# Kernel tuning notes

Measured on AMD Instinct MI355X. Metric: run time of the kernel, lower is better.

## Reference

```python
import jax, jax.numpy as jnp
import numpy as np

F = 128          # feature_size
N = 512          # num_vertices (batch_size fixed to 1 by the original indexing)
C = 32 * 7 * 7 * 7   # 10976, f2 channel dim
G = 13           # f2 spatial grid (indices = (v+1)*6 in [0,12])
EPS = 1e-5


def _block(x, W1, b1, W2, b2, g, be, m, v):
    # Linear -> ELU -> Linear -> ELU -> Dropout(eval=id) -> BatchNorm1d(eval)
    h = jax.nn.elu(x @ W1 + b1)
    h = jax.nn.elu(h @ W2 + b2)
    return (h - m) * (g * jax.lax.rsqrt(v + EPS)) + be


def setup_inputs() -> dict:
    key = jax.random.key(0)
    ks = iter(jax.random.split(key, 80))

    def nrm(sh, s):
        return jax.random.normal(next(ks), sh, jnp.float32) * s

    def lin(i, o):
        return nrm((i, o), 1.0 / np.sqrt(i)), nrm((o,), 0.01)

    def bn():
        g = 1.0 + nrm((F,), 0.05)
        be = nrm((F,), 0.05)
        m = nrm((F,), 0.1)
        v = jax.random.uniform(next(ks), (F,), jnp.float32) + 0.5
        return g, be, m, v

    d = {}
    d['vertices'] = jax.random.uniform(next(ks), (1, N, 3), jnp.float32) * 2.0 - 1.0
    d['f2'] = nrm((1, G, G, G, C), 0.1)
    ii = jnp.arange(N, dtype=jnp.int32)
    d['v1s_idx'] = jnp.repeat(ii, N)   # edge k=(i,j): i = k//N
    d['v2s_idx'] = jnp.tile(ii, N)     #               j = k%N
    d['adj'] = (jax.random.uniform(next(ks), (N, N)) < 0.05).astype(jnp.float32)

    for p, (i, o) in [('mv', (3, F)), ('mf', (C, F)), ('s1', (2 * F, F)),
                      ('s2', (F, F)), ('s3', (2 * F, F))]:
        W1, b1 = lin(i, o)
        W2, b2 = lin(F, F)
        g, be, m, v = bn()
        d.update({p + '_W1': W1, p + '_b1': b1, p + '_W2': W2, p + '_b2': b2,
                  p + '_g': g, p + '_be': be, p + '_m': m, p + '_v': v})
    W3, b3 = lin(F, 2)
    d['s3_W3'], d['s3_b3'] = W3, b3
    return d


def _forward(vertices, f2, adj,
             mv_W1, mv_b1, mv_W2, mv_b2, mv_g, mv_be, mv_m, mv_v,
             mf_W1, mf_b1, mf_W2, mf_b2, mf_g, mf_be, mf_m, mf_v,
             s1_W1, s1_b1, s1_W2, s1_b2, s1_g, s1_be, s1_m, s1_v,
             s2_W1, s2_b1, s2_W2, s2_b2, s2_g, s2_be, s2_m, s2_v,
             s3_W1, s3_b1, s3_W2, s3_b2, s3_g, s3_be, s3_m, s3_v, s3_W3, s3_b3,
             v1s_idx, v2s_idx):
    b, n, _ = vertices.shape
    flat = vertices.reshape(-1, 3)                        # (B*N, 3)
    idx = ((flat + 1.0) * 6.0).astype(jnp.int32)          # grid indices in [0,12]
    f2e = f2[0, idx[:, 0], idx[:, 1], idx[:, 2], :]       # gather: (B*N, C)
    vf = _block(flat, mv_W1, mv_b1, mv_W2, mv_b2, mv_g, mv_be, mv_m, mv_v)
    ff = _block(f2e, mf_W1, mf_b1, mf_W2, mf_b2, mf_g, mf_be, mf_m, mf_v)
    vert = jnp.concatenate([vf, ff], -1).reshape(b, n, 2 * F)  # (B, N, 2F)

    # stage1: NodeToEdge (endpoint combine) -> MLP block over all N^2 edges
    e1 = vert[:, v1s_idx] + vert[:, v2s_idx]              # (B, N*N, 2F)
    s1 = _block(e1, s1_W1, s1_b1, s1_W2, s1_b2, s1_g, s1_be, s1_m, s1_v)  # (B, E, F)

    # stage2: EdgeToNode (adjacency-masked sum) -> MLP -> NodeToEdge
    nodes = jnp.einsum('bijf,ij->bif', s1.reshape(b, n, n, F), adj)  # (B, N, F)
    n2 = _block(nodes, s2_W1, s2_b1, s2_W2, s2_b2, s2_g, s2_be, s2_m, s2_v)
    s2 = n2[:, v1s_idx] + n2[:, v2s_idx]                  # (B, E, F)

    cat = jnp.concatenate([s1, s2], -1).reshape(b * n * n, 2 * F)
    h = _block(cat, s3_W1, s3_b1, s3_W2, s3_b2, s3_g, s3_be, s3_m, s3_v)
    return (h @ s3_W3 + s3_b3).reshape(b, n, n, 2)


def reference(vertices, f2, v1s_idx, v2s_idx, adj,
              mv_W1, mv_b1, mv_W2, mv_b2, mv_g, mv_be, mv_m, mv_v,
              mf_W1, mf_b1, mf_W2, mf_b2, mf_g, mf_be, mf_m, mf_v,
              s1_W1, s1_b1, s1_W2, s1_b2, s1_g, s1_be, s1_m, s1_v,
              s2_W1, s2_b1, s2_W2, s2_b2, s2_g, s2_be, s2_m, s2_v,
              s3_W1, s3_b1, s3_W2, s3_b2, s3_g, s3_be, s3_m, s3_v, s3_W3, s3_b3):
    return _forward(vertices, f2, adj,
                    mv_W1, mv_b1, mv_W2, mv_b2, mv_g, mv_be, mv_m, mv_v,
                    mf_W1, mf_b1, mf_W2, mf_b2, mf_g, mf_be, mf_m, mf_v,
                    s1_W1, s1_b1, s1_W2, s1_b2, s1_g, s1_be, s1_m, s1_v,
                    s2_W1, s2_b1, s2_W2, s2_b2, s2_g, s2_be, s2_m, s2_v,
                    s3_W1, s3_b1, s3_W2, s3_b2, s3_g, s3_be, s3_m, s3_v, s3_W3, s3_b3,
                    v1s_idx, v2s_idx)
```

## Files before the change

kernel.cpp:

```cpp
#include <hip/hip_runtime.h>
#include <hip/hip_bf16.h>


#define F    128
#define NV   512
#define CCC  10976
#define EPSV 1e-5f

typedef __attribute__((ext_vector_type(8)))  short        short8;
typedef __attribute__((ext_vector_type(4)))  float        f32x4;
typedef __attribute__((ext_vector_type(4)))  float        flt4;
typedef __attribute__((ext_vector_type(4)))  unsigned int u32x4;

union Frag { u32x4 q; short8 s; unsigned int d[4]; unsigned short u[8]; };

__device__ __forceinline__ unsigned short f2bf(float x){
  union { float f; unsigned int u; } c; c.f = x;
  unsigned int r = c.u + 0x7FFFu + ((c.u >> 16) & 1u);
  return (unsigned short)(r >> 16);
}
__device__ __forceinline__ unsigned int pkbf(float a, float b){
  union { __hip_bfloat162 h; unsigned int u; } cv;
  cv.h = __float22bfloat162_rn(make_float2(a, b));
  return cv.u;
}
__device__ __forceinline__ float eluf(float x){
  return x > 0.f ? x : (__expf(x) - 1.f);
}
__device__ __forceinline__ f32x4 mfma16(short8 a, short8 b, f32x4 c){
  return __builtin_amdgcn_mfma_f32_16x16x32_bf16(a, b, c, 0, 0, 0);
}

#define WS_U      0u
#define WS_FFPRE  262144u
#define WS_WPERM  524288u
#define WS_CTR    786432u
#define WS_VEC    794624u
#define WS_W2FS1  799744u
#define WS_W1AFS3 832512u
#define WS_W2FS3  865280u
#define WS_W3F    898048u
#define WS_MFW1F  902144u
#define WS_END    3712000u
#define WS_PART   3712000u
#define WS_PART_END 14984192u


#define NJOBS   4352
#define NSTATIC 4096

__global__ __launch_bounds__(256) void k_setup(
    const float* s1W2, const float* s3W1, const float* s3W2, const float* s3W3,
    const float* __restrict__ mfW1,
    const float* s1g, const float* s1v,
    const float* s3g, const float* s3be, const float* s3m, const float* s3v,
    const float* s1be, const float* s1m,
    const float* s1b2, const float* s3b2,
    unsigned short* w2fs1, unsigned short* w1afs3, unsigned short* w2fs3,
    unsigned short* w3f, unsigned short* __restrict__ mfw1f,
    float* vec, float* zeroreg, unsigned int* ctr, int use_parts)
{
  __shared__ float sm[32 * 132];
  int bid = blockIdx.x, tid = threadIdx.x;
  if (bid == 0 && tid < 8) ctr[tid * 256] = 0u;

  if (bid < 460){
    int t = bid * 256 + tid;
    if (t < 49152){
      int T = t >> 14, tt = t & 16383;
      int e = tt & 7, lane = (tt >> 3) & 63, grp = tt >> 9;
      int slot = (grp >> 3) * 32 + ((lane >> 4) & 3) * 8 + e;
      int col  = (grp & 7) * 16 + (lane & 15);
      float val;
      unsigned short* dst;
      if (T == 0){ dst = w2fs1; val = s1W2[slot * F + col]; }
      else {
        int kf = (slot & 7) * 16 + (slot >> 3);
        if (T == 1){
          float sc1 = s1g[kf] * rsqrtf(s1v[kf] + EPSV);
          dst = w1afs3; val = sc1 * s3W1[kf * F + col];
        } else {
          dst = w2fs3; val = s3W2[kf * F + col];
        }
      }
      dst[tt] = f2bf(val);
      return;
    }
    t -= 49152;
    if (t < 2048){
      int e = t & 7, lane = (t >> 3) & 63, ks = t >> 9;
      int slot = ks * 32 + ((lane >> 4) & 3) * 8 + e;
      int kf = (slot & 7) * 16 + (slot >> 3);
      int n = lane & 15;
      float sc3 = s3g[kf] * rsqrtf(s3v[kf] + EPSV);
      w3f[t] = f2bf(n < 2 ? sc3 * s3W3[kf * 2 + n] : 0.f);
      return;
    }
    t -= 2048;
    if (t < 1024){
      int f = t & 127, which = t >> 7;
      int s = (f & 15) * 8 + (f >> 4);
      switch (which){
        case 0: vec[512 + s] = s1b2[f]; break;
        case 1: vec[640 + s] = s3b2[f]; break;
        case 2: vec[768 + f] = s1g[f] * rsqrtf(s1v[f] + EPSV); break;
        case 3: vec[896 + f] = s1be[f] - s1m[f] * (s1g[f] * rsqrtf(s1v[f] + EPSV)); break;
        case 4: {
          float a = 0.f;
          for (int k = 0; k < F; ++k){
            float sc = s1g[k] * rsqrtf(s1v[k] + EPSV);
            a = fmaf(s1be[k] - s1m[k] * sc, s3W1[k * F + f], a);
          }
          vec[1024 + f] = a;
        } break;
        case 5: if (f < 16){
          float a = 0.f;
          if (f < 2){
            for (int k = 0; k < F; ++k){
              float sc = s3g[k] * rsqrtf(s3v[k] + EPSV);
              a = fmaf(s3be[k] - s3m[k] * sc, s3W3[k * 2 + f], a);
            }
          }
          vec[1152 + f] = a;
        } break;
        default: break;
      }
      return;
    }
    t -= 1024;
    if (t < 65536 && !use_parts) zeroreg[t] = 0.f;
    return;
  }

  {
    int ksg = bid - 460;
    const float* src = mfW1 + ksg * 32 * F;
    #pragma unroll
    for (int p = 0; p < 4; ++p){
      int g4 = tid + p * 256;
      int row = g4 >> 5, col = (g4 & 31) * 4;
      flt4 v = *(const flt4*)(src + row * F + col);
      *(flt4*)(sm + row * 132 + col) = v;
    }
    __syncthreads();
    unsigned int* dst = (unsigned int*)mfw1f + ksg * 2048;
    #pragma unroll
    for (int q2 = 0; q2 < 8; ++q2){
      int o = (tid * 8 + q2) * 2;
      int nt = o >> 9, lane = (o >> 3) & 63, e = o & 7;
      int k = (lane >> 4) * 8 + e;
      int n = nt * 16 + (lane & 15);
      dst[tid * 8 + q2] = pkbf(sm[k * 132 + n], sm[(k + 1) * 132 + n]);
    }
  }
}

__global__ __launch_bounds__(256) void k_ff1(
    const float* __restrict__ verts, const float* __restrict__ f2,
    const unsigned short* __restrict__ mfw1f, float* __restrict__ ffpre,
    float* __restrict__ partials, int use_parts)
{
  int tid = threadIdx.x, w = tid >> 6, l = tid & 63, g = l >> 4, mm = l & 15;
  int mb = blockIdx.x & 7, kc = blockIdx.x >> 3;
  int v = mb * 64 + w * 16 + mm;
  float x0 = verts[v * 3 + 0], x1 = verts[v * 3 + 1], x2 = verts[v * 3 + 2];
  int i0 = (int)((x0 + 1.f) * 6.f), i1 = (int)((x1 + 1.f) * 6.f), i2 = (int)((x2 + 1.f) * 6.f);
  int base = ((i0 * 13 + i1) * 13 + i2) * CCC;

  f32x4 zero = {0.f, 0.f, 0.f, 0.f};
  f32x4 acc[8];
  #pragma unroll
  for (int nt = 0; nt < 8; ++nt) acc[nt] = zero;

  const u32x4* bt = (const u32x4*)mfw1f;
  int kmax = 343 - kc * 8; if (kmax > 8) kmax = 8;
  for (int kk = 0; kk < kmax; ++kk){
    int ksg = kc * 8 + kk;
    const float* ap = f2 + base + ksg * 32 + g * 8;
    flt4 a0 = *(const flt4*)ap;
    flt4 a1 = *(const flt4*)(ap + 4);
    Frag a;
    a.d[0] = pkbf(a0.x, a0.y); a.d[1] = pkbf(a0.z, a0.w);
    a.d[2] = pkbf(a1.x, a1.y); a.d[3] = pkbf(a1.z, a1.w);
    #pragma unroll
    for (int nt = 0; nt < 8; ++nt){
      Frag b; b.q = bt[(ksg * 8 + nt) * 64 + l];
      acc[nt] = mfma16(a.s, b.s, acc[nt]);
    }
  }
  if (use_parts){
    #pragma unroll
    for (int nt = 0; nt < 8; ++nt){
      int n = nt * 16 + mm;
      #pragma unroll
      for (int r = 0; r < 4; ++r)
        partials[(kc * NV + mb * 64 + w * 16 + g * 4 + r) * F + n] = acc[nt][r];
    }
  } else {
    #pragma unroll
    for (int nt = 0; nt < 8; ++nt){
      int n = nt * 16 + mm;
      #pragma unroll
      for (int r = 0; r < 4; ++r)
        atomicAdd(&ffpre[(mb * 64 + w * 16 + g * 4 + r) * F + n], acc[nt][r]);
    }
  }
}

__global__ __launch_bounds__(256) void k_vert(
    const float* __restrict__ verts, const float* __restrict__ ffpre,
    const float* __restrict__ partials, int use_parts,
    const float* mvW1, const float* mvb1, const float* mvW2, const float* mvb2,
    const float* mvg, const float* mvbe, const float* mvm, const float* mvv,
    const float* mfb1, const float* mfW2, const float* mfb2,
    const float* mfg, const float* mfbe, const float* mfm, const float* mfv,
    const float* s1W1, const float* s1b1, float* __restrict__ uP)
{
  __shared__ float hv[F], hf[F], vf[F], ff[F], ph0[F], ph1[F];
  int tid = threadIdx.x, f = tid & 127, half = tid >> 7, v = blockIdx.x;
  if (half == 0){
    float x0 = verts[v * 3], x1 = verts[v * 3 + 1], x2 = verts[v * 3 + 2];
    hv[f] = eluf(mvb1[f] + x0 * mvW1[f] + x1 * mvW1[F + f] + x2 * mvW1[2 * F + f]);
  } else {
    float fp;
    if (use_parts){
      fp = 0.f;
      for (int kc = 0; kc < 43; ++kc) fp += partials[(kc * NV + v) * F + f];
    } else {
      fp = ffpre[v * F + f];
    }
    hf[f] = eluf(fp + mfb1[f]);
  }
  __syncthreads();
  {
    float psv = 0.f, psf = 0.f;
    const float* wv_ = mvW2 + half * 64 * F + f;
    const float* wf_ = mfW2 + half * 64 * F + f;
    const float* hvk = hv + half * 64;
    const float* hfk = hf + half * 64;
    for (int k = 0; k < 64; ++k){
      psv = fmaf(hvk[k], wv_[k * F], psv);
      psf = fmaf(hfk[k], wf_[k * F], psf);
    }
    if (half){ ph0[f] = psv; ph1[f] = psf; }
    __syncthreads();
    if (!half){
      float sv = mvb2[f] + psv + ph0[f];
      float sf = mfb2[f] + psf + ph1[f];
      vf[f] = (eluf(sv) - mvm[f]) * (mvg[f] * rsqrtf(mvv[f] + EPSV)) + mvbe[f];
      ff[f] = (eluf(sf) - mfm[f]) * (mfg[f] * rsqrtf(mfv[f] + EPSV)) + mfbe[f];
    }
    __syncthreads();
  }
  {
    float pu = 0.f;
    if (half == 0){
      for (int k = 0; k < F; ++k) pu = fmaf(vf[k], s1W1[k * F + f], pu);
    } else {
      for (int k = 0; k < F; ++k) pu = fmaf(ff[k], s1W1[(128 + k) * F + f], pu);
    }
    if (half) ph0[f] = pu;
    __syncthreads();
    if (!half) uP[v * F + f] = 0.5f * s1b1[f] + pu + ph0[f];
  }
}

__global__ __launch_bounds__(256) void k_pass1m(
    const float* __restrict__ uP, const unsigned short* __restrict__ w2fs1,
    const float* __restrict__ vec, const float* __restrict__ adj,
    const float* s2W1, const float* s2b1, const float* s2W2, const float* s2b2,
    const float* s2g, const float* s2be, const float* s2m, const float* s2v,
    const float* s3W1, const float* s3b1, float* __restrict__ wPp)
{
  __shared__ u32x4 Wb[2048];
  __shared__ float ci[F], nblk[F], bb[F], mh0[F];
  __shared__ unsigned short pjl[128];
  __shared__ unsigned long long msk[8];
  int tid = threadIdx.x, i = blockIdx.x;
  int wv = tid >> 6, ln = tid & 63;

  bool p0 = adj[i * NV + tid] != 0.f;
  bool p1 = adj[i * NV + 256 + tid] != 0.f;
  unsigned long long m0 = __ballot(p0);
  unsigned long long m1 = __ballot(p1);
  if (ln == 0){ msk[wv] = m0; msk[4 + wv] = m1; }
  { const u32x4* ws_ = (const u32x4*)w2fs1;
    #pragma unroll
    for (int ii = 0; ii < 8; ++ii) Wb[tid + 256 * ii] = ws_[tid + 256 * ii]; }
  if (tid < F){ ci[tid] = uP[i * F + tid]; nblk[tid] = 0.f; }
  __syncthreads();
  int base0 = 0, base1 = 0, tot = 0;
  #pragma unroll
  for (int g = 0; g < 8; ++g){
    int c = __popcll(msk[g]);
    if (g < wv) base0 += c;
    if (g < 4 + wv) base1 += c;
    tot += c;
  }
  unsigned long long below = (1ull << ln) - 1ull;
  if (p0){
    int r = base0 + __popcll(m0 & below);
    if (r < 128) pjl[r] = (unsigned short)tid;
  }
  if (p1){
    int r = base1 + __popcll(m1 & below);
    if (r < 128) pjl[r] = (unsigned short)(256 + tid);
  }
  int cnt = tot > 128 ? 128 : tot;
  float cntf = (float)tot;
  __syncthreads();

  int w = tid >> 6, l = tid & 63, g = l >> 4, mm = l & 15;
  float b2v[8];
  *(flt4*)&b2v[0] = *(const flt4*)(vec + 512 + mm * 8);
  *(flt4*)&b2v[4] = *(const flt4*)(vec + 516 + mm * 8);

  for (int t = 0; t * 64 < cnt; ++t){
    int row = t * 64 + w * 16 + mm;
    int j = (row < cnt) ? (int)pjl[row] : 0;
    f32x4 acc[8];
    #pragma unroll
    for (int nt = 0; nt < 8; ++nt){ float b = b2v[nt]; acc[nt] = (f32x4){b, b, b, b}; }
    #pragma unroll
    for (int ks = 0; ks < 4; ++ks){
      int kb = ks * 32 + g * 8;
      flt4 ua = *(const flt4*)(uP + j * F + kb);
      flt4 ub = *(const flt4*)(uP + j * F + kb + 4);
      flt4 c0 = *(const flt4*)&ci[kb];
      flt4 c1 = *(const flt4*)&ci[kb + 4];
      Frag a;
      a.d[0] = pkbf(eluf(ua.x + c0.x), eluf(ua.y + c0.y));
      a.d[1] = pkbf(eluf(ua.z + c0.z), eluf(ua.w + c0.w));
      a.d[2] = pkbf(eluf(ub.x + c1.x), eluf(ub.y + c1.y));
      a.d[3] = pkbf(eluf(ub.z + c1.z), eluf(ub.w + c1.w));
      #pragma unroll
      for (int nt = 0; nt < 8; ++nt){
        Frag b; b.q = Wb[(ks * 8 + nt) * 64 + l];
        acc[nt] = mfma16(a.s, b.s, acc[nt]);
      }
    }
    int rbase = t * 64 + w * 16 + g * 4;
    float mk[4];
    #pragma unroll
    for (int r = 0; r < 4; ++r) mk[r] = (rbase + r < cnt) ? 1.f : 0.f;
    #pragma unroll
    for (int nt = 0; nt < 8; ++nt){
      float s = mk[0] * eluf(acc[nt][0]);
      s = fmaf(mk[1], eluf(acc[nt][1]), s);
      s = fmaf(mk[2], eluf(acc[nt][2]), s);
      s = fmaf(mk[3], eluf(acc[nt][3]), s);
      s += __shfl_xor(s, 16, 64);
      s += __shfl_xor(s, 32, 64);
      if (l < 16) atomicAdd(&nblk[nt * 16 + mm], s);
    }
  }
  __syncthreads();

  if (tid < F) ci[tid] = vec[768 + tid] * nblk[tid] + vec[896 + tid] * cntf;
  __syncthreads();
  int f = tid & 127, half = tid >> 7;
  {
    float p = 0.f;
    const float* Wc = s2W1 + half * 64 * F + f;
    const float* av = ci + half * 64;
    for (int k = 0; k < 64; ++k) p = fmaf(av[k], Wc[k * F], p);
    if (half) mh0[f] = p;
    __syncthreads();
    if (!half) bb[f] = eluf(s2b1[f] + p + mh0[f]);
    __syncthreads();
  }
  {
    float p = 0.f;
    const float* Wc = s2W2 + half * 64 * F + f;
    const float* av = bb + half * 64;
    for (int k = 0; k < 64; ++k) p = fmaf(av[k], Wc[k * F], p);
    if (half) mh0[f] = p;
    __syncthreads();
    if (!half){
      float s2 = s2b2[f] + p + mh0[f];
      nblk[f] = (eluf(s2) - s2m[f]) * (s2g[f] * rsqrtf(s2v[f] + EPSV)) + s2be[f];
    }
    __syncthreads();
  }
  {
    float p = 0.f;
    const float* Wc = s3W1 + (128 + half * 64) * F + f;
    const float* av = nblk + half * 64;
    for (int k = 0; k < 64; ++k) p = fmaf(av[k], Wc[k * F], p);
    if (half) mh0[f] = p;
    __syncthreads();
    if (!half){
      float wvv = 0.5f * (s3b1[f] + vec[1024 + f]) + p + mh0[f];
      wPp[i * F + ((f & 15) * 8 + (f >> 4))] = wvv;
    }
  }
}

__global__ __launch_bounds__(512, 2) void k_pass3(
    const float* __restrict__ uP, const float* __restrict__ wPp,
    const unsigned short* __restrict__ w2fs1, const unsigned short* __restrict__ w1afs3,
    const unsigned short* __restrict__ w2fs3, const unsigned short* __restrict__ w3f,
    const float* __restrict__ vec, const float* __restrict__ s3b3,
    unsigned int* __restrict__ ctr, float* __restrict__ out)
{
  __shared__ u32x4 Wall[6144];
  __shared__ __align__(16) char Hb[65536];
  int tid = threadIdx.x;
  {
    const u32x4* p0 = (const u32x4*)w2fs1;
    const u32x4* p1 = (const u32x4*)w1afs3;
    const u32x4* p2 = (const u32x4*)w2fs3;
    #pragma unroll
    for (int ii = 0; ii < 4; ++ii){
      Wall[       tid + 512 * ii] = p0[tid + 512 * ii];
      Wall[2048 + tid + 512 * ii] = p1[tid + 512 * ii];
      Wall[4096 + tid + 512 * ii] = p2[tid + 512 * ii];
    }
  }
  __syncthreads();

  int w = tid >> 6, l = tid & 63, g = l >> 4, mm = l & 15;
  char* hb = Hb + w * 8192;
  int sx = (mm & 7) << 4;
  int wgid = blockIdx.x * 8 + w;
  unsigned int* ctrp = ctr + (blockIdx.x & 7) * 256;
  int cgrp = blockIdx.x & 7;

  float b2v1[8], b2v3[8];
  *(flt4*)&b2v1[0] = *(const flt4*)(vec + 512 + mm * 8);
  *(flt4*)&b2v1[4] = *(const flt4*)(vec + 516 + mm * 8);
  *(flt4*)&b2v3[0] = *(const flt4*)(vec + 640 + mm * 8);
  *(flt4*)&b2v3[4] = *(const flt4*)(vec + 644 + mm * 8);
  float bb = (mm < 2) ? (s3b3[mm] + vec[1152 + mm]) : 0.f;
  Frag w3r[4];
  #pragma unroll
  for (int ks = 0; ks < 4; ++ks) w3r[ks].q = ((const u32x4*)w3f)[ks * 64 + l];

  int phase = 0;
  for (;;){
    int id;
    if (phase < 2){
      id = wgid * 2 + phase;
      ++phase;
    } else {
      int t;
      if (l == 0) t = (int)atomicAdd(ctrp, 1u);
      t = __shfl(t, 0, 64);
      if (t >= 32) break;
      id = NSTATIC + cgrp * 32 + t;
    }
    int q = (id >= 512) + (id >= 992) + (id >= 1440) + (id >= 1856)
          + (id >= 2240) + (id >= 2592) + (id >= 2912) + (id >= 3200)
          + (id >= 3456) + (id >= 3680) + (id >= 3872) + (id >= 4032)
          + (id >= 4160) + (id >= 4256) + (id >= 4320);
    int Sq = 32 * (16 * q - ((q * (q - 1)) >> 1));
    int r_ = id - Sq;
    int den = 16 - q;
    int i = q * 32 + r_ / den;
    int jbase = 32 * (q + r_ % den);

    flt4 c0[4], c1[4];
    #pragma unroll
    for (int ks = 0; ks < 4; ++ks){
      c0[ks] = *(const flt4*)(uP + i * F + ks * 32 + g * 8);
      c1[ks] = *(const flt4*)(uP + i * F + ks * 32 + g * 8 + 4);
    }

    f32x4 acc[2][8];
    #pragma unroll
    for (int m = 0; m < 2; ++m)
    #pragma unroll
    for (int nt = 0; nt < 8; ++nt){ float b = b2v1[nt]; acc[m][nt] = (f32x4){b, b, b, b}; }
    #pragma unroll
    for (int ks = 0; ks < 4; ++ks){
      int kb = ks * 32 + g * 8;
      Frag a0, a1;
      {
        const float* p0 = uP + (jbase + mm) * F + kb;
        flt4 ua = *(const flt4*)p0;
        flt4 ub = *(const flt4*)(p0 + 4);
        a0.d[0] = pkbf(eluf(ua.x + c0[ks].x), eluf(ua.y + c0[ks].y));
        a0.d[1] = pkbf(eluf(ua.z + c0[ks].z), eluf(ua.w + c0[ks].w));
        a0.d[2] = pkbf(eluf(ub.x + c1[ks].x), eluf(ub.y + c1[ks].y));
        a0.d[3] = pkbf(eluf(ub.z + c1[ks].z), eluf(ub.w + c1[ks].w));
        const float* p1 = uP + (jbase + 16 + mm) * F + kb;
        flt4 va = *(const flt4*)p1;
        flt4 vb = *(const flt4*)(p1 + 4);
        a1.d[0] = pkbf(eluf(va.x + c0[ks].x), eluf(va.y + c0[ks].y));
        a1.d[1] = pkbf(eluf(va.z + c0[ks].z), eluf(va.w + c0[ks].w));
        a1.d[2] = pkbf(eluf(vb.x + c1[ks].x), eluf(vb.y + c1[ks].y));
        a1.d[3] = pkbf(eluf(vb.z + c1[ks].z), eluf(vb.w + c1[ks].w));
      }
      #pragma unroll
      for (int nt = 0; nt < 8; ++nt){
        Frag b; b.q = Wall[(ks * 8 + nt) * 64 + l];
        acc[0][nt] = mfma16(a0.s, b.s, acc[0][nt]);
        acc[1][nt] = mfma16(a1.s, b.s, acc[1][nt]);
      }
    }
    #pragma unroll
    for (int m = 0; m < 2; ++m)
    #pragma unroll
    for (int r = 0; r < 4; ++r){
      int row = m * 16 + g * 4 + r;
      u32x4 wd;
      #pragma unroll
      for (int qq = 0; qq < 4; ++qq)
        wd[qq] = pkbf(eluf(acc[m][2*qq][r]), eluf(acc[m][2*qq+1][r]));
      *(u32x4*)(hb + row * 256 + ((mm * 16) ^ ((row & 7) << 4))) = wd;
    }

    {
      float wiv[8];
      *(flt4*)&wiv[0] = *(const flt4*)(wPp + i * F + mm * 8);
      *(flt4*)&wiv[4] = *(const flt4*)(wPp + i * F + mm * 8 + 4);
      #pragma unroll
      for (int m = 0; m < 2; ++m)
      #pragma unroll
      for (int nt = 0; nt < 8; ++nt){ float b = wiv[nt]; acc[m][nt] = (f32x4){b, b, b, b}; }
    }
    #pragma unroll
    for (int ks = 0; ks < 4; ++ks){
      Frag a0; a0.q = *(const u32x4*)(hb + mm * 256 + ((ks * 64 + g * 16) ^ sx));
      Frag a1; a1.q = *(const u32x4*)(hb + (16 + mm) * 256 + ((ks * 64 + g * 16) ^ sx));
      #pragma unroll
      for (int nt = 0; nt < 8; ++nt){
        Frag b; b.q = Wall[2048 + (ks * 8 + nt) * 64 + l];
        acc[0][nt] = mfma16(a0.s, b.s, acc[0][nt]);
        acc[1][nt] = mfma16(a1.s, b.s, acc[1][nt]);
      }
    }
    #pragma unroll
    for (int m = 0; m < 2; ++m)
    #pragma unroll
    for (int r = 0; r < 4; ++r){
      int row = m * 16 + g * 4 + r;
      int jj = jbase + row;
      float wjv[8];
      *(flt4*)&wjv[0] = *(const flt4*)(wPp + jj * F + mm * 8);
      *(flt4*)&wjv[4] = *(const flt4*)(wPp + jj * F + mm * 8 + 4);
      u32x4 wd;
      #pragma unroll
      for (int qq = 0; qq < 4; ++qq)
        wd[qq] = pkbf(eluf(acc[m][2*qq][r] + wjv[2*qq]), eluf(acc[m][2*qq+1][r] + wjv[2*qq+1]));
      *(u32x4*)(hb + row * 256 + ((mm * 16) ^ ((row & 7) << 4))) = wd;
    }

    #pragma unroll
    for (int m = 0; m < 2; ++m)
    #pragma unroll
    for (int nt = 0; nt < 8; ++nt){ float b = b2v3[nt]; acc[m][nt] = (f32x4){b, b, b, b}; }
    #pragma unroll
    for (int ks = 0; ks < 4; ++ks){
      Frag a0; a0.q = *(const u32x4*)(hb + mm * 256 + ((ks * 64 + g * 16) ^ sx));
      Frag a1; a1.q = *(const u32x4*)(hb + (16 + mm) * 256 + ((ks * 64 + g * 16) ^ sx));
      #pragma unroll
      for (int nt = 0; nt < 8; ++nt){
        Frag b; b.q = Wall[4096 + (ks * 8 + nt) * 64 + l];
        acc[0][nt] = mfma16(a0.s, b.s, acc[0][nt]);
        acc[1][nt] = mfma16(a1.s, b.s, acc[1][nt]);
      }
    }
    #pragma unroll
    for (int m = 0; m < 2; ++m)
    #pragma unroll
    for (int r = 0; r < 4; ++r){
      int row = m * 16 + g * 4 + r;
      u32x4 wd;
      #pragma unroll
      for (int qq = 0; qq < 4; ++qq)
        wd[qq] = pkbf(eluf(acc[m][2*qq][r]), eluf(acc[m][2*qq+1][r]));
      *(u32x4*)(hb + row * 256 + ((mm * 16) ^ ((row & 7) << 4))) = wd;
    }

    f32x4 acc4[2] = {{bb, bb, bb, bb}, {bb, bb, bb, bb}};
    #pragma unroll
    for (int ks = 0; ks < 4; ++ks){
      Frag a0; a0.q = *(const u32x4*)(hb + mm * 256 + ((ks * 64 + g * 16) ^ sx));
      Frag a1; a1.q = *(const u32x4*)(hb + (16 + mm) * 256 + ((ks * 64 + g * 16) ^ sx));
      acc4[0] = mfma16(a0.s, w3r[ks].s, acc4[0]);
      acc4[1] = mfma16(a1.s, w3r[ks].s, acc4[1]);
    }
    if (mm < 2){
      #pragma unroll
      for (int m = 0; m < 2; ++m)
      #pragma unroll
      for (int r = 0; r < 4; ++r){
        int jr = jbase + m * 16 + g * 4 + r;
        if (jr >= i){
          float val = acc4[m][r];
          out[(i * NV + jr) * 2 + mm] = val;
          out[(jr * NV + i) * 2 + mm] = val;
        }
      }
    }
  }
}

extern "C" void kernel_launch(void* const* d_in, const int* in_sizes, int n_in,
                              void* d_out, int out_size, void* d_ws, size_t ws_size,
                              hipStream_t stream)
{
  (void)in_sizes; (void)n_in; (void)out_size;
  const float* vertices = (const float*)d_in[0];
  const float* f2   = (const float*)d_in[1];
  const float* adj  = (const float*)d_in[4];
  const float* mvW1 = (const float*)d_in[5];
  const float* mvb1 = (const float*)d_in[6];
  const float* mvW2 = (const float*)d_in[7];
  const float* mvb2 = (const float*)d_in[8];
  const float* mvg  = (const float*)d_in[9];
  const float* mvbe = (const float*)d_in[10];
  const float* mvm  = (const float*)d_in[11];
  const float* mvv  = (const float*)d_in[12];
  const float* mfW1 = (const float*)d_in[13];
  const float* mfb1 = (const float*)d_in[14];
  const float* mfW2 = (const float*)d_in[15];
  const float* mfb2 = (const float*)d_in[16];
  const float* mfg  = (const float*)d_in[17];
  const float* mfbe = (const float*)d_in[18];
  const float* mfm  = (const float*)d_in[19];
  const float* mfv  = (const float*)d_in[20];
  const float* s1W1 = (const float*)d_in[21];
  const float* s1b1 = (const float*)d_in[22];
  const float* s1W2 = (const float*)d_in[23];
  const float* s1b2 = (const float*)d_in[24];
  const float* s1g  = (const float*)d_in[25];
  const float* s1be = (const float*)d_in[26];
  const float* s1m  = (const float*)d_in[27];
  const float* s1v  = (const float*)d_in[28];
  const float* s2W1 = (const float*)d_in[29];
  const float* s2b1 = (const float*)d_in[30];
  const float* s2W2 = (const float*)d_in[31];
  const float* s2b2 = (const float*)d_in[32];
  const float* s2g  = (const float*)d_in[33];
  const float* s2be = (const float*)d_in[34];
  const float* s2m  = (const float*)d_in[35];
  const float* s2v  = (const float*)d_in[36];
  const float* s3W1 = (const float*)d_in[37];
  const float* s3b1 = (const float*)d_in[38];
  const float* s3W2 = (const float*)d_in[39];
  const float* s3b2 = (const float*)d_in[40];
  const float* s3g  = (const float*)d_in[41];
  const float* s3be = (const float*)d_in[42];
  const float* s3m  = (const float*)d_in[43];
  const float* s3v  = (const float*)d_in[44];
  const float* s3W3 = (const float*)d_in[45];
  const float* s3b3 = (const float*)d_in[46];

  char* ws = (char*)d_ws;
  float* uP    = (float*)(ws + WS_U);
  float* ffpre = (float*)(ws + WS_FFPRE);
  float* wPp   = (float*)(ws + WS_WPERM);
  unsigned int* ctr = (unsigned int*)(ws + WS_CTR);
  float* vec   = (float*)(ws + WS_VEC);
  unsigned short* w2fs1  = (unsigned short*)(ws + WS_W2FS1);
  unsigned short* w1afs3 = (unsigned short*)(ws + WS_W1AFS3);
  unsigned short* w2fs3  = (unsigned short*)(ws + WS_W2FS3);
  unsigned short* w3f    = (unsigned short*)(ws + WS_W3F);
  unsigned short* mfw1f  = (unsigned short*)(ws + WS_MFW1F);
  float* parts = (float*)(ws + WS_PART);
  int use_parts = (ws_size >= (size_t)WS_PART_END) ? 1 : 0;

  k_setup<<<803, 256, 0, stream>>>(s1W2, s3W1, s3W2, s3W3, mfW1,
      s1g, s1v, s3g, s3be, s3m, s3v, s1be, s1m, s1b2, s3b2,
      w2fs1, w1afs3, w2fs3, w3f, mfw1f, vec, ffpre, ctr, use_parts);
  k_ff1<<<344, 256, 0, stream>>>(vertices, f2, mfw1f, ffpre, parts, use_parts);
  k_vert<<<512, 256, 0, stream>>>(vertices, ffpre, parts, use_parts,
      mvW1, mvb1, mvW2, mvb2, mvg, mvbe, mvm, mvv,
      mfb1, mfW2, mfb2, mfg, mfbe, mfm, mfv,
      s1W1, s1b1, uP);
  k_pass1m<<<512, 256, 0, stream>>>(uP, w2fs1, vec, adj,
      s2W1, s2b1, s2W2, s2b2, s2g, s2be, s2m, s2v, s3W1, s3b1, wPp);
  k_pass3<<<256, 512, 0, stream>>>(uP, wPp, w2fs1, w1afs3, w2fs3, w3f, vec,
      s3b3, ctr, (float*)d_out);
}
```

Before: 95.27 us.

## Fuse mfW1 bf16 conversion into ff1 and shrink pass3 tiles to 16 rows

```diff
diff --git a/kernel.cpp b/kernel.cpp
--- a/kernel.cpp
+++ b/kernel.cpp
@@ -40,126 +40,99 @@
 #define WS_W1AFS3 832512u
 #define WS_W2FS3  865280u
 #define WS_W3F    898048u
-#define WS_MFW1F  902144u
-#define WS_END    3712000u
-#define WS_PART   3712000u
-#define WS_PART_END 14984192u
-
-
-#define NJOBS   4352
-#define NSTATIC 4096
+#define WS_END    902144u
+#define WS_PART   902144u
+#define WS_PART_END 12174336u
+
+
+#define NJOBS16   8448
+#define NSTATIC16 6144
 
 __global__ __launch_bounds__(256) void k_setup(
     const float* s1W2, const float* s3W1, const float* s3W2, const float* s3W3,
-    const float* __restrict__ mfW1,
     const float* s1g, const float* s1v,
     const float* s3g, const float* s3be, const float* s3m, const float* s3v,
     const float* s1be, const float* s1m,
     const float* s1b2, const float* s3b2,
     unsigned short* w2fs1, unsigned short* w1afs3, unsigned short* w2fs3,
-    unsigned short* w3f, unsigned short* __restrict__ mfw1f,
-    float* vec, float* zeroreg, unsigned int* ctr, int use_parts)
+    unsigned short* w3f, float* vec, float* zeroreg, unsigned int* ctr,
+    int use_parts)
+{
+  int bid = blockIdx.x, tid = threadIdx.x;
+  if (bid == 0 && tid < 8) ctr[tid * 256] = 0u;
+
+  int t = bid * 256 + tid;
+  if (t < 49152){
+    int T = t >> 14, tt = t & 16383;
+    int e = tt & 7, lane = (tt >> 3) & 63, grp = tt >> 9;
+    int slot = (grp >> 3) * 32 + ((lane >> 4) & 3) * 8 + e;
+    int col  = (grp & 7) * 16 + (lane & 15);
+    float val;
+    unsigned short* dst;
+    if (T == 0){ dst = w2fs1; val = s1W2[slot * F + col]; }
+    else {
+      int kf = (slot & 7) * 16 + (slot >> 3);
+      if (T == 1){
+        float sc1 = s1g[kf] * rsqrtf(s1v[kf] + EPSV);
+        dst = w1afs3; val = sc1 * s3W1[kf * F + col];
+      } else {
+        dst = w2fs3; val = s3W2[kf * F + col];
+      }
+    }
+    dst[tt] = f2bf(val);
+    return;
+  }
+  t -= 49152;
+  if (t < 2048){
+    int e = t & 7, lane = (t >> 3) & 63, ks = t >> 9;
+    int slot = ks * 32 + ((lane >> 4) & 3) * 8 + e;
+    int kf = (slot & 7) * 16 + (slot >> 3);
+    int n = lane & 15;
+    float sc3 = s3g[kf] * rsqrtf(s3v[kf] + EPSV);
+    w3f[t] = f2bf(n < 2 ? sc3 * s3W3[kf * 2 + n] : 0.f);
+    return;
+  }
+  t -= 2048;
+  if (t < 1024){
+    int f = t & 127, which = t >> 7;
+    int s = (f & 15) * 8 + (f >> 4);
+    switch (which){
+      case 0: vec[512 + s] = s1b2[f]; break;
+      case 1: vec[640 + s] = s3b2[f]; break;
+      case 2: vec[768 + f] = s1g[f] * rsqrtf(s1v[f] + EPSV); break;
+      case 3: vec[896 + f] = s1be[f] - s1m[f] * (s1g[f] * rsqrtf(s1v[f] + EPSV)); break;
+      case 4: {
+        float a = 0.f;
+        for (int k = 0; k < F; ++k){
+          float sc = s1g[k] * rsqrtf(s1v[k] + EPSV);
+          a = fmaf(s1be[k] - s1m[k] * sc, s3W1[k * F + f], a);
+        }
+        vec[1024 + f] = a;
+      } break;
+      case 5: if (f < 16){
+        float a = 0.f;
+        if (f < 2){
+          for (int k = 0; k < F; ++k){
+            float sc = s3g[k] * rsqrtf(s3v[k] + EPSV);
+            a = fmaf(s3be[k] - s3m[k] * sc, s3W3[k * 2 + f], a);
+          }
+        }
+        vec[1152 + f] = a;
+      } break;
+      default: break;
+    }
+    return;
+  }
+  t -= 1024;
+  if (t < 65536 && !use_parts) zeroreg[t] = 0.f;
+}
+
+__global__ __launch_bounds__(256) void k_ff1(
+    const float* __restrict__ verts, const float* __restrict__ f2,
+    const float* __restrict__ mfW1, float* __restrict__ ffpre,
+    float* __restrict__ partials, int use_parts)
 {
   __shared__ float sm[32 * 132];
-  int bid = blockIdx.x, tid = threadIdx.x;
-  if (bid == 0 && tid < 8) ctr[tid * 256] = 0u;
-
-  if (bid < 460){
-    int t = bid * 256 + tid;
-    if (t < 49152){
-      int T = t >> 14, tt = t & 16383;
-      int e = tt & 7, lane = (tt >> 3) & 63, grp = tt >> 9;
-      int slot = (grp >> 3) * 32 + ((lane >> 4) & 3) * 8 + e;
-      int col  = (grp & 7) * 16 + (lane & 15);
-      float val;
-      unsigned short* dst;
-      if (T == 0){ dst = w2fs1; val = s1W2[slot * F + col]; }
-      else {
-        int kf = (slot & 7) * 16 + (slot >> 3);
-        if (T == 1){
-          float sc1 = s1g[kf] * rsqrtf(s1v[kf] + EPSV);
-          dst = w1afs3; val = sc1 * s3W1[kf * F + col];
-        } else {
-          dst = w2fs3; val = s3W2[kf * F + col];
-        }
-      }
-      dst[tt] = f2bf(val);
-      return;
-    }
-    t -= 49152;
-    if (t < 2048){
-      int e = t & 7, lane = (t >> 3) & 63, ks = t >> 9;
-      int slot = ks * 32 + ((lane >> 4) & 3) * 8 + e;
-      int kf = (slot & 7) * 16 + (slot >> 3);
-      int n = lane & 15;
-      float sc3 = s3g[kf] * rsqrtf(s3v[kf] + EPSV);
-      w3f[t] = f2bf(n < 2 ? sc3 * s3W3[kf * 2 + n] : 0.f);
-      return;
-    }
-    t -= 2048;
-    if (t < 1024){
-      int f = t & 127, which = t >> 7;
-      int s = (f & 15) * 8 + (f >> 4);
-      switch (which){
-        case 0: vec[512 + s] = s1b2[f]; break;
-        case 1: vec[640 + s] = s3b2[f]; break;
-        case 2: vec[768 + f] = s1g[f] * rsqrtf(s1v[f] + EPSV); break;
-        case 3: vec[896 + f] = s1be[f] - s1m[f] * (s1g[f] * rsqrtf(s1v[f] + EPSV)); break;
-        case 4: {
-          float a = 0.f;
-          for (int k = 0; k < F; ++k){
-            float sc = s1g[k] * rsqrtf(s1v[k] + EPSV);
-            a = fmaf(s1be[k] - s1m[k] * sc, s3W1[k * F + f], a);
-          }
-          vec[1024 + f] = a;
-        } break;
-        case 5: if (f < 16){
-          float a = 0.f;
-          if (f < 2){
-            for (int k = 0; k < F; ++k){
-              float sc = s3g[k] * rsqrtf(s3v[k] + EPSV);
-              a = fmaf(s3be[k] - s3m[k] * sc, s3W3[k * 2 + f], a);
-            }
-          }
-          vec[1152 + f] = a;
-        } break;
-        default: break;
-      }
-      return;
-    }
-    t -= 1024;
-    if (t < 65536 && !use_parts) zeroreg[t] = 0.f;
-    return;
-  }
-
-  {
-    int ksg = bid - 460;
-    const float* src = mfW1 + ksg * 32 * F;
-    #pragma unroll
-    for (int p = 0; p < 4; ++p){
-      int g4 = tid + p * 256;
-      int row = g4 >> 5, col = (g4 & 31) * 4;
-      flt4 v = *(const flt4*)(src + row * F + col);
-      *(flt4*)(sm + row * 132 + col) = v;
-    }
-    __syncthreads();
-    unsigned int* dst = (unsigned int*)mfw1f + ksg * 2048;
-    #pragma unroll
-    for (int q2 = 0; q2 < 8; ++q2){
-      int o = (tid * 8 + q2) * 2;
-      int nt = o >> 9, lane = (o >> 3) & 63, e = o & 7;
-      int k = (lane >> 4) * 8 + e;
-      int n = nt * 16 + (lane & 15);
-      dst[tid * 8 + q2] = pkbf(sm[k * 132 + n], sm[(k + 1) * 132 + n]);
-    }
-  }
-}
-
-__global__ __launch_bounds__(256) void k_ff1(
-    const float* __restrict__ verts, const float* __restrict__ f2,
-    const unsigned short* __restrict__ mfw1f, float* __restrict__ ffpre,
-    float* __restrict__ partials, int use_parts)
-{
   int tid = threadIdx.x, w = tid >> 6, l = tid & 63, g = l >> 4, mm = l & 15;
   int mb = blockIdx.x & 7, kc = blockIdx.x >> 3;
   int v = mb * 64 + w * 16 + mm;
@@ -172,10 +145,19 @@
   #pragma unroll
   for (int nt = 0; nt < 8; ++nt) acc[nt] = zero;
 
-  const u32x4* bt = (const u32x4*)mfw1f;
   int kmax = 343 - kc * 8; if (kmax > 8) kmax = 8;
+  int k0 = g * 8;
   for (int kk = 0; kk < kmax; ++kk){
     int ksg = kc * 8 + kk;
+    const float* src = mfW1 + ksg * 32 * F;
+    #pragma unroll
+    for (int p = 0; p < 4; ++p){
+      int g4 = tid + p * 256;
+      int row = g4 >> 5, col = (g4 & 31) * 4;
+      flt4 vv = *(const flt4*)(src + row * F + col);
+      *(flt4*)(sm + row * 132 + col) = vv;
+    }
+    __syncthreads();
     const float* ap = f2 + base + ksg * 32 + g * 8;
     flt4 a0 = *(const flt4*)ap;
     flt4 a1 = *(const flt4*)(ap + 4);
@@ -184,9 +166,14 @@
     a.d[2] = pkbf(a1.x, a1.y); a.d[3] = pkbf(a1.z, a1.w);
     #pragma unroll
     for (int nt = 0; nt < 8; ++nt){
-      Frag b; b.q = bt[(ksg * 8 + nt) * 64 + l];
+      int n = nt * 16 + mm;
+      Frag b;
+      #pragma unroll
+      for (int j = 0; j < 4; ++j)
+        b.d[j] = pkbf(sm[(k0 + 2 * j) * 132 + n], sm[(k0 + 2 * j + 1) * 132 + n]);
       acc[nt] = mfma16(a.s, b.s, acc[nt]);
     }
+    __syncthreads();
   }
   if (use_parts){
     #pragma unroll
@@ -396,7 +383,7 @@
   }
 }
 
-__global__ __launch_bounds__(512, 2) void k_pass3(
+__global__ __launch_bounds__(768, 3) void k_pass3(
     const float* __restrict__ uP, const float* __restrict__ wPp,
     const unsigned short* __restrict__ w2fs1, const unsigned short* __restrict__ w1afs3,
     const unsigned short* __restrict__ w2fs3, const unsigned short* __restrict__ w3f,
@@ -404,25 +391,28 @@
     unsigned int* __restrict__ ctr, float* __restrict__ out)
 {
   __shared__ u32x4 Wall[6144];
-  __shared__ __align__(16) char Hb[65536];
+  __shared__ __align__(16) char Hb[49152];
   int tid = threadIdx.x;
   {
     const u32x4* p0 = (const u32x4*)w2fs1;
     const u32x4* p1 = (const u32x4*)w1afs3;
     const u32x4* p2 = (const u32x4*)w2fs3;
     #pragma unroll
-    for (int ii = 0; ii < 4; ++ii){
-      Wall[       tid + 512 * ii] = p0[tid + 512 * ii];
-      Wall[2048 + tid + 512 * ii] = p1[tid + 512 * ii];
-      Wall[4096 + tid + 512 * ii] = p2[tid + 512 * ii];
+    for (int ii = 0; ii < 3; ++ii){
+      int idx = tid + 768 * ii;
+      if (idx < 2048){
+        Wall[idx]        = p0[idx];
+        Wall[2048 + idx] = p1[idx];
+        Wall[4096 + idx] = p2[idx];
+      }
     }
   }
   __syncthreads();
 
   int w = tid >> 6, l = tid & 63, g = l >> 4, mm = l & 15;
-  char* hb = Hb + w * 8192;
+  char* hb = Hb + w * 4096;
   int sx = (mm & 7) << 4;
-  int wgid = blockIdx.x * 8 + w;
+  int wgid = blockIdx.x * 12 + w;
   unsigned int* ctrp = ctr + (blockIdx.x & 7) * 256;
   int cgrp = blockIdx.x & 7;
 
@@ -431,7 +421,7 @@
   *(flt4*)&b2v1[4] = *(const flt4*)(vec + 516 + mm * 8);
   *(flt4*)&b2v3[0] = *(const flt4*)(vec + 640 + mm * 8);
   *(flt4*)&b2v3[4] = *(const flt4*)(vec + 644 + mm * 8);
-  float bb = (mm < 2) ? (s3b3[mm] + vec[1152 + mm]) : 0.f;
+  float bbc = (mm < 2) ? (s3b3[mm] + vec[1152 + mm]) : 0.f;
   Frag w3r[4];
   #pragma unroll
   for (int ks = 0; ks < 4; ++ks) w3r[ks].q = ((const u32x4*)w3f)[ks * 64 + l];
@@ -446,149 +436,132 @@
       int t;
       if (l == 0) t = (int)atomicAdd(ctrp, 1u);
       t = __shfl(t, 0, 64);
-      if (t >= 32) break;
-      id = NSTATIC + cgrp * 32 + t;
-    }
-    int q = (id >= 512) + (id >= 992) + (id >= 1440) + (id >= 1856)
-          + (id >= 2240) + (id >= 2592) + (id >= 2912) + (id >= 3200)
-          + (id >= 3456) + (id >= 3680) + (id >= 3872) + (id >= 4032)
-          + (id >= 4160) + (id >= 4256) + (id >= 4320);
-    int Sq = 32 * (16 * q - ((q * (q - 1)) >> 1));
-    int r_ = id - Sq;
-    int den = 16 - q;
-    int i = q * 32 + r_ / den;
-    int jbase = 32 * (q + r_ % den);
-
-    flt4 c0[4], c1[4];
+      if (t >= 288) break;
+      id = NSTATIC16 + cgrp * 288 + t;
+    }
+    int gq = (int)((65.0f - sqrtf(4225.0f - 0.5f * (float)id)) * 0.5f);
+    if (gq < 0) gq = 0; if (gq > 31) gq = 31;
+    while (gq < 31 && 8 * (gq + 1) * (65 - (gq + 1)) <= id) ++gq;
+    while (gq > 0 && 8 * gq * (65 - gq) > id) --gq;
+    int r_ = id - 8 * gq * (65 - gq);
+    int den = 32 - gq;
+    int i = gq * 16 + r_ / den;
+    int jbase = 16 * (gq + r_ % den);
+
+    flt4 c0[4], c1[4], u0[4], u1[4];
     #pragma unroll
     for (int ks = 0; ks < 4; ++ks){
       c0[ks] = *(const flt4*)(uP + i * F + ks * 32 + g * 8);
       c1[ks] = *(const flt4*)(uP + i * F + ks * 32 + g * 8 + 4);
-    }
-
-    f32x4 acc[2][8];
-    #pragma unroll
-    for (int m = 0; m < 2; ++m)
-    #pragma unroll
-    for (int nt = 0; nt < 8; ++nt){ float b = b2v1[nt]; acc[m][nt] = (f32x4){b, b, b, b}; }
+      const float* pA = uP + (jbase + mm) * F + ks * 32 + g * 8;
+      u0[ks] = *(const flt4*)pA;
+      u1[ks] = *(const flt4*)(pA + 4);
+    }
+
+    f32x4 acc[8];
+    #pragma unroll
+    for (int nt = 0; nt < 8; ++nt){ float b = b2v1[nt]; acc[nt] = (f32x4){b, b, b, b}; }
     #pragma unroll
     for (int ks = 0; ks < 4; ++ks){
-      int kb = ks * 32 + g * 8;
-      Frag a0, a1;
-      {
-        const float* p0 = uP + (jbase + mm) * F + kb;
-        flt4 ua = *(const flt4*)p0;
-        flt4 ub = *(const flt4*)(p0 + 4);
-        a0.d[0] = pkbf(eluf(ua.x + c0[ks].x), eluf(ua.y + c0[ks].y));
-        a0.d[1] = pkbf(eluf(ua.z + c0[ks].z), eluf(ua.w + c0[ks].w));
-        a0.d[2] = pkbf(eluf(ub.x + c1[ks].x), eluf(ub.y + c1[ks].y));
-        a0.d[3] = pkbf(eluf(ub.z + c1[ks].z), eluf(ub.w + c1[ks].w));
-        const float* p1 = uP + (jbase + 16 + mm) * F + kb;
-        flt4 va = *(const flt4*)p1;
-        flt4 vb = *(const flt4*)(p1 + 4);
-        a1.d[0] = pkbf(eluf(va.x + c0[ks].x), eluf(va.y + c0[ks].y));
-        a1.d[1] = pkbf(eluf(va.z + c0[ks].z), eluf(va.w + c0[ks].w));
-        a1.d[2] = pkbf(eluf(vb.x + c1[ks].x), eluf(vb.y + c1[ks].y));
-        a1.d[3] = pkbf(eluf(vb.z + c1[ks].z), eluf(vb.w + c1[ks].w));
-      }
+      Frag a;
+      a.d[0] = pkbf(eluf(u0[ks].x + c0[ks].x), eluf(u0[ks].y + c0[ks].y));
+      a.d[1] = pkbf(eluf(u0[ks].z + c0[ks].z), eluf(u0[ks].w + c0[ks].w));
+      a.d[2] = pkbf(eluf(u1[ks].x + c1[ks].x), eluf(u1[ks].y + c1[ks].y));
+      a.d[3] = pkbf(eluf(u1[ks].z + c1[ks].z), eluf(u1[ks].w + c1[ks].w));
       #pragma unroll
       for (int nt = 0; nt < 8; ++nt){
         Frag b; b.q = Wall[(ks * 8 + nt) * 64 + l];
-        acc[0][nt] = mfma16(a0.s, b.s, acc[0][nt]);
-        acc[1][nt] = mfma16(a1.s, b.s, acc[1][nt]);
-      }
-    }
-    #pragma unroll
-    for (int m = 0; m < 2; ++m)
+        acc[nt] = mfma16(a.s, b.s, acc[nt]);
+      }
+    }
     #pragma unroll
     for (int r = 0; r < 4; ++r){
-      int row = m * 16 + g * 4 + r;
+      int row = g * 4 + r;
       u32x4 wd;
       #pragma unroll
       for (int qq = 0; qq < 4; ++qq)
-        wd[qq] = pkbf(eluf(acc[m][2*qq][r]), eluf(acc[m][2*qq+1][r]));
+        wd[qq] = pkbf(eluf(acc[2*qq][r]), eluf(acc[2*qq+1][r]));
       *(u32x4*)(hb + row * 256 + ((mm * 16) ^ ((row & 7) << 4))) = wd;
     }
 
     {
+      Frag sA[4];
+      #pragma unroll
+      for (int ks = 0; ks < 4; ++ks)
+        sA[ks].q = *(const u32x4*)(hb + mm * 256 + ((ks * 64 + g * 16) ^ sx));
       float wiv[8];
       *(flt4*)&wiv[0] = *(const flt4*)(wPp + i * F + mm * 8);
       *(flt4*)&wiv[4] = *(const flt4*)(wPp + i * F + mm * 8 + 4);
-      #pragma unroll
-      for (int m = 0; m < 2; ++m)
-      #pragma unroll
-      for (int nt = 0; nt < 8; ++nt){ float b = wiv[nt]; acc[m][nt] = (f32x4){b, b, b, b}; }
-    }
-    #pragma unroll
-    for (int ks = 0; ks < 4; ++ks){
-      Frag a0; a0.q = *(const u32x4*)(hb + mm * 256 + ((ks * 64 + g * 16) ^ sx));
-      Frag a1; a1.q = *(const u32x4*)(hb + (16 + mm) * 256 + ((ks * 64 + g * 16) ^ sx));
-      #pragma unroll
-      for (int nt = 0; nt < 8; ++nt){
-        Frag b; b.q = Wall[2048 + (ks * 8 + nt) * 64 + l];
-        acc[0][nt] = mfma16(a0.s, b.s, acc[0][nt]);
-        acc[1][nt] = mfma16(a1.s, b.s, acc[1][nt]);
-      }
-    }
-    #pragma unroll
-    for (int m = 0; m < 2; ++m)
-    #pragma unroll
-    for (int r = 0; r < 4; ++r){
-      int row = m * 16 + g * 4 + r;
-      int jj = jbase + row;
-      float wjv[8];
-      *(flt4*)&wjv[0] = *(const flt4*)(wPp + jj * F + mm * 8);
-      *(flt4*)&wjv[4] = *(const flt4*)(wPp + jj * F + mm * 8 + 4);
-      u32x4 wd;
-      #pragma unroll
-      for (int qq = 0; qq < 4; ++qq)
-        wd[qq] = pkbf(eluf(acc[m][2*qq][r] + wjv[2*qq]), eluf(acc[m][2*qq+1][r] + wjv[2*qq+1]));
-      *(u32x4*)(hb + row * 256 + ((mm * 16) ^ ((row & 7) << 4))) = wd;
-    }
-
-    #pragma unroll
-    for (int m = 0; m < 2; ++m)
-    #pragma unroll
-    for (int nt = 0; nt < 8; ++nt){ float b = b2v3[nt]; acc[m][nt] = (f32x4){b, b, b, b}; }
-    #pragma unroll
-    for (int ks = 0; ks < 4; ++ks){
-      Frag a0; a0.q = *(const u32x4*)(hb + mm * 256 + ((ks * 64 + g * 16) ^ sx));
-      Frag a1; a1.q = *(const u32x4*)(hb + (16 + mm) * 256 + ((ks * 64 + g * 16) ^ sx));
-      #pragma unroll
-      for (int nt = 0; nt < 8; ++nt){
-        Frag b; b.q = Wall[4096 + (ks * 8 + nt) * 64 + l];
-        acc[0][nt] = mfma16(a0.s, b.s, acc[0][nt]);
-        acc[1][nt] = mfma16(a1.s, b.s, acc[1][nt]);
-      }
-    }
-    #pragma unroll
-    for (int m = 0; m < 2; ++m)
-    #pragma unroll
-    for (int r = 0; r < 4; ++r){
-      int row = m * 16 + g * 4 + r;
-      u32x4 wd;
-      #pragma unroll
-      for (int qq = 0; qq < 4; ++qq)
-        wd[qq] = pkbf(eluf(acc[m][2*qq][r]), eluf(acc[m][2*qq+1][r]));
-      *(u32x4*)(hb + row * 256 + ((mm * 16) ^ ((row & 7) << 4))) = wd;
-    }
-
-    f32x4 acc4[2] = {{bb, bb, bb, bb}, {bb, bb, bb, bb}};
-    #pragma unroll
-    for (int ks = 0; ks < 4; ++ks){
-      Frag a0; a0.q = *(const u32x4*)(hb + mm * 256 + ((ks * 64 + g * 16) ^ sx));
-      Frag a1; a1.q = *(const u32x4*)(hb + (16 + mm) * 256 + ((ks * 64 + g * 16) ^ sx));
-      acc4[0] = mfma16(a0.s, w3r[ks].s, acc4[0]);
-      acc4[1] = mfma16(a1.s, w3r[ks].s, acc4[1]);
+      float wj[4][8];
+      #pragma unroll
+      for (int r = 0; r < 4; ++r){
+        int jj = jbase + g * 4 + r;
+        *(flt4*)&wj[r][0] = *(const flt4*)(wPp + jj * F + mm * 8);
+        *(flt4*)&wj[r][4] = *(const flt4*)(wPp + jj * F + mm * 8 + 4);
+      }
+      #pragma unroll
+      for (int nt = 0; nt < 8; ++nt){ float b = wiv[nt]; acc[nt] = (f32x4){b, b, b, b}; }
+      #pragma unroll
+      for (int ks = 0; ks < 4; ++ks){
+        #pragma unroll
+        for (int nt = 0; nt < 8; ++nt){
+          Frag b; b.q = Wall[2048 + (ks * 8 + nt) * 64 + l];
+          acc[nt] = mfma16(sA[ks].s, b.s, acc[nt]);
+        }
+      }
+      #pragma unroll
+      for (int r = 0; r < 4; ++r){
+        int row = g * 4 + r;
+        u32x4 wd;
+        #pragma unroll
+        for (int qq = 0; qq < 4; ++qq)
+          wd[qq] = pkbf(eluf(acc[2*qq][r] + wj[r][2*qq]), eluf(acc[2*qq+1][r] + wj[r][2*qq+1]));
+        *(u32x4*)(hb + row * 256 + ((mm * 16) ^ ((row & 7) << 4))) = wd;
+      }
+    }
+
+    {
+      Frag sA[4];
+      #pragma unroll
+      for (int ks = 0; ks < 4; ++ks)
+        sA[ks].q = *(const u32x4*)(hb + mm * 256 + ((ks * 64 + g * 16) ^ sx));
+      #pragma unroll
+      for (int nt = 0; nt < 8; ++nt){ float b = b2v3[nt]; acc[nt] = (f32x4){b, b, b, b}; }
+      #pragma unroll
+      for (int ks = 0; ks < 4; ++ks){
+        #pragma unroll
+        for (int nt = 0; nt < 8; ++nt){
+          Frag b; b.q = Wall[4096 + (ks * 8 + nt) * 64 + l];
+          acc[nt] = mfma16(sA[ks].s, b.s, acc[nt]);
+        }
+      }
+      #pragma unroll
+      for (int r = 0; r < 4; ++r){
+        int row = g * 4 + r;
+        u32x4 wd;
+        #pragma unroll
+        for (int qq = 0; qq < 4; ++qq)
+          wd[qq] = pkbf(eluf(acc[2*qq][r]), eluf(acc[2*qq+1][r]));
+        *(u32x4*)(hb + row * 256 + ((mm * 16) ^ ((row & 7) << 4))) = wd;
+      }
+    }
+
+    f32x4 acc4 = {bbc, bbc, bbc, bbc};
+    {
+      Frag sA[4];
+      #pragma unroll
+      for (int ks = 0; ks < 4; ++ks)
+        sA[ks].q = *(const u32x4*)(hb + mm * 256 + ((ks * 64 + g * 16) ^ sx));
+      #pragma unroll
+      for (int ks = 0; ks < 4; ++ks)
+        acc4 = mfma16(sA[ks].s, w3r[ks].s, acc4);
     }
     if (mm < 2){
       #pragma unroll
-      for (int m = 0; m < 2; ++m)
-      #pragma unroll
       for (int r = 0; r < 4; ++r){
-        int jr = jbase + m * 16 + g * 4 + r;
+        int jr = jbase + g * 4 + r;
         if (jr >= i){
-          float val = acc4[m][r];
+          float val = acc4[r];
           out[(i * NV + jr) * 2 + mm] = val;
           out[(jr * NV + i) * 2 + mm] = val;
         }
@@ -658,20 +631,20 @@
   unsigned short* w1afs3 = (unsigned short*)(ws + WS_W1AFS3);
   unsigned short* w2fs3  = (unsigned short*)(ws + WS_W2FS3);
   unsigned short* w3f    = (unsigned short*)(ws + WS_W3F);
-  unsigned short* mfw1f  = (unsigned short*)(ws + WS_MFW1F);
   float* parts = (float*)(ws + WS_PART);
   int use_parts = (ws_size >= (size_t)WS_PART_END) ? 1 : 0;
-
-  k_setup<<<803, 256, 0, stream>>>(s1W2, s3W1, s3W2, s3W3, mfW1,
+  int prep_blocks = use_parts ? 204 : 460;
+
+  k_setup<<<prep_blocks, 256, 0, stream>>>(s1W2, s3W1, s3W2, s3W3,
       s1g, s1v, s3g, s3be, s3m, s3v, s1be, s1m, s1b2, s3b2,
-      w2fs1, w1afs3, w2fs3, w3f, mfw1f, vec, ffpre, ctr, use_parts);
-  k_ff1<<<344, 256, 0, stream>>>(vertices, f2, mfw1f, ffpre, parts, use_parts);
+      w2fs1, w1afs3, w2fs3, w3f, vec, ffpre, ctr, use_parts);
+  k_ff1<<<344, 256, 0, stream>>>(vertices, f2, mfW1, ffpre, parts, use_parts);
   k_vert<<<512, 256, 0, stream>>>(vertices, ffpre, parts, use_parts,
       mvW1, mvb1, mvW2, mvb2, mvg, mvbe, mvm, mvv,
       mfb1, mfW2, mfb2, mfg, mfbe, mfm, mfv,
       s1W1, s1b1, uP);
   k_pass1m<<<512, 256, 0, stream>>>(uP, w2fs1, vec, adj,
       s2W1, s2b1, s2W2, s2b2, s2g, s2be, s2m, s2v, s3W1, s3b1, wPp);
-  k_pass3<<<256, 512, 0, stream>>>(uP, wPp, w2fs1, w1afs3, w2fs3, w3f, vec,
+  k_pass3<<<256, 768, 0, stream>>>(uP, wPp, w2fs1, w1afs3, w2fs3, w3f, vec,
       s3b3, ctr, (float*)d_out);
 }
```

After: 102.1 us. +7.2%, slower.
